# Optimization experiments

Hardware: AMD Instinct MI355X
Metric: run time of the kernel (lower is better)

Reference implementation:

```python
import jax, jax.numpy as jnp
import numpy as np
from jax import lax

EPS = 2.220446049250313e-16  # np.finfo(float).eps, as in the torch source
DN3 = ('NCDHW', 'OIDHW', 'NCDHW')
DN2 = ('NCHW', 'OIHW', 'NCHW')


def setup_inputs() -> dict:
    key = jax.random.key(0)
    k1, k2, k3 = jax.random.split(key, 3)
    x = jax.random.normal(k1, (256, 256), dtype=jnp.float32)
    filts_temp = jax.random.normal(k2, (8, 1, 2, 9, 9), dtype=jnp.float32)    # [Ft,1,T=2,kh,kw]
    filts_notemp = jax.random.normal(k3, (8, 1, 1, 9, 9), dtype=jnp.float32)  # [Fn,1,1,kh,kw]
    return {"x": x, "filts_temp": filts_temp, "filts_notemp": filts_notemp, "num_rfs": 2}


def _forward(x, filts_temp, filts_notemp, num_rfs):
    kh, kw = filts_temp.shape[3], filts_temp.shape[4]
    corr_x = num_rfs * kh  # torch uses shape[3]
    corr_y = num_rfs * kw  # torch uses shape[4]
    num_filts = filts_temp.shape[0] + filts_notemp.shape[0]

    # x -> [1,1,2,H,W]: duplicate the frame along a temporal axis of length 2
    xv = jnp.broadcast_to(x, (2,) + x.shape)[None, None]

    # fixed-filter temporal conv3d + ReLU (halved)
    x_temp = jax.nn.relu(
        lax.conv_general_dilated(xv, filts_temp, (1, 1, 1), 'VALID', dimension_numbers=DN3) / 2
    )  # [1,Ft,1,H',W']
    # non-temporal conv on the last time slice
    x_notemp = jax.nn.relu(
        lax.conv_general_dilated(xv[:, :, -1:, :, :], filts_notemp, (1, 1, 1), 'VALID',
                                 dimension_numbers=DN3)
    )  # [1,Fn,1,H',W']

    xc = jnp.concatenate([x_temp, x_notemp], axis=1)  # [1,nf,1,H',W']
    # normalize across the filter channel (divisive normalization)
    x1 = xc / (jnp.sum(xc, axis=1, keepdims=True) + EPS)

    H_, W_ = x1.shape[3], x1.shape[4]
    x1f = x1[0, :, 0]  # [nf,H',W']
    # central crop used as correlation templates
    templates = x1f[:, corr_y:H_ - corr_y, corr_x:W_ - corr_x]  # [nf, H'-2cy, W'-2cx]

    # windowed pairwise cross-channel correlation: the torch conv3d with depth-kernel 1
    # is exactly a batched 2D valid cross-correlation (batch = depth index j,
    # out-channel = template index i)
    out = lax.conv_general_dilated(x1f[:, None], templates[:, None], (1, 1), 'VALID',
                                   dimension_numbers=DN2)  # [j, i, 2cy+1, 2cx+1]
    x2 = jnp.transpose(out, (1, 0, 2, 3))[None]  # [1, i, j, 2cy+1, 2cx+1]
    # note: source divides by (y_max-2*corr_y)*(x_max-2*corr_y) (corr_y twice) -- kept faithful
    x2 = x2 / ((H_ - 2 * corr_y) * (W_ - 2 * corr_y))

    x1_out = x1f[None, None]  # [1,1,nf,H',W']
    return (x1_out, x2)


def reference(x, filts_temp, filts_notemp, num_rfs):
    return _forward(x, filts_temp, filts_notemp, num_rfs)
```

## Files before the change

kernel.cpp:

```cpp
#include <hip/hip_runtime.h>
#include <hip/hip_fp8.h>
#include <cstdint>

typedef unsigned short u16;
typedef unsigned int   u32;
typedef unsigned long long u64;
typedef float  f32x16 __attribute__((ext_vector_type(16)));
typedef float  f32x4  __attribute__((ext_vector_type(4)));
typedef u32    u32x2  __attribute__((ext_vector_type(2)));
typedef u32    u32x4  __attribute__((ext_vector_type(4)));

#define OUT1 984064
#define OUT2 350464

#define XD5        1015808
#define TMPL_OFFB  16252928
#define PART_OFFB  17027072
#define PART_ELEMS (6*OUT2)
#define XC_OFFB    25438208

__global__ __launch_bounds__(256) void k1_conv(
    const float* __restrict__ x, const float* __restrict__ ft,
    const float* __restrict__ fnt, float* __restrict__ out1,
    u16* __restrict__ Xc) {
  __shared__ float xt[24][25];
  __shared__ float wsm[1296];
  const int tid = threadIdx.x;
  const int lx = tid & 15, ly = tid >> 4;
  const int bx = blockIdx.x, by = blockIdx.y;
  for (int idx = tid; idx < 1296; idx += 256) {
    int c = idx / 81, s = idx - (idx / 81) * 81;
    wsm[idx] = (c < 8) ? 0.5f * (ft[c*162 + s] + ft[c*162 + 81 + s])
                       : fnt[(c-8)*81 + s];
  }
  for (int idx = tid; idx < 576; idx += 256) {
    int ry = idx / 24, rx = idx - ry * 24;
    int gy = by*16 + ry; gy = gy > 255 ? 255 : gy;
    int gx = bx*16 + rx; gx = gx > 255 ? 255 : gx;
    xt[ry][rx] = x[gy*256 + gx];
  }
  __syncthreads();
  const int xg = bx*16 + lx, yg = by*16 + ly;
  if (yg >= 248) return;
  float s[16];
#pragma unroll
  for (int c = 0; c < 16; ++c) s[c] = 0.f;
  const bool valid = (xg < 248);
  if (valid) {
#pragma unroll
    for (int u = 0; u < 9; ++u)
#pragma unroll
      for (int v = 0; v < 9; ++v) {
        float xv = xt[ly + u][lx + v];
#pragma unroll
        for (int c = 0; c < 16; ++c)
          s[c] = __builtin_fmaf(xv, wsm[c*81 + u*9 + v], s[c]);
      }
    float sum = 2.2204460492503131e-16f;
#pragma unroll
    for (int c = 0; c < 16; ++c) { s[c] = s[c] > 0.f ? s[c] : 0.f; sum += s[c]; }
    float inv = 1.f / sum;
#pragma unroll
    for (int c = 0; c < 16; ++c) s[c] *= inv;
  }
#pragma unroll
  for (int c = 0; c < 16; ++c) {
    u16 hb = 0;
    if (valid) {
      out1[c*61504 + yg*248 + xg] = s[c];
      u32 ub = __builtin_bit_cast(u32, s[c]);
      hb = (u16)((ub + 0x7fffu + ((ub >> 16) & 1u)) >> 16);
    }
    Xc[(c*248 + yg)*272 + xg] = hb;
  }
}

__device__ __forceinline__ u32 pk4_fp8(u32 b0, u32 b1) {
  float f0 = __builtin_bit_cast(float, b0 << 16);
  float f1 = __builtin_bit_cast(float, b0 & 0xFFFF0000u);
  float f2 = __builtin_bit_cast(float, b1 << 16);
  float f3 = __builtin_bit_cast(float, b1 & 0xFFFF0000u);
  __hip_fp8_e4m3 e0(f0), e1(f1), e2(f2), e3(f3);
  return (u32)e0.__x | ((u32)e1.__x << 8) | ((u32)e2.__x << 16) | ((u32)e3.__x << 24);
}

__global__ __launch_bounds__(256) void k1b_expand(
    const u16* __restrict__ Xc, unsigned char* __restrict__ ws8,
    float* __restrict__ partial) {
  const int cid = blockIdx.x*256 + threadIdx.x;
  for (int z = cid; z < PART_ELEMS; z += gridDim.x*256) partial[z] = 0.f;
  const u32* src = (const u32*)Xc;
  if (cid < 1015808) {
    int n  = cid & 15;
    int r1 = cid >> 4;
    int row = r1 % 248;
    int r2  = r1 / 248;
    int vp  = r2 & 15;
    int d   = r2 >> 4;
    int col0 = d + 16*vp;
    int so = (n*248 + row)*136 + (col0 >> 1);
    u32 a[9], b[8];
#pragma unroll
    for (int i = 0; i < 9; ++i) a[i] = src[so + i];
    if (d & 1) {
#pragma unroll
      for (int i = 0; i < 8; ++i) b[i] = (a[i] >> 16) | (a[i+1] << 16);
    } else {
#pragma unroll
      for (int i = 0; i < 8; ++i) b[i] = a[i];
    }
    u32x4 v = { pk4_fp8(b[0], b[1]), pk4_fp8(b[2], b[3]),
                pk4_fp8(b[4], b[5]), pk4_fp8(b[6], b[7]) };
    *(u32x4*)(ws8 + ((size_t)((d*16 + vp)*248 + row))*256 + n*16) = v;
  } else if (cid < 1015808 + 48384) {
    int t  = cid - 1015808;
    int o  = t & 15;
    int r1 = t >> 4;
    int tr = r1 % 216;
    int vp = r1 / 216;
    u32x4 v = {0u, 0u, 0u, 0u};
    if (tr < 212) {
      int so = (o*248 + tr + 18)*136 + ((18 + 16*vp) >> 1);
      u32 b[8];
#pragma unroll
      for (int i = 0; i < 8; ++i) b[i] = src[so + i];
      v[0] = pk4_fp8(b[0], b[1]);
      if (vp < 13) {
        v[1] = pk4_fp8(b[2], b[3]);
        v[2] = pk4_fp8(b[4], b[5]);
        v[3] = pk4_fp8(b[6], b[7]);
      }
    }
    *(u32x4*)(ws8 + TMPL_OFFB + ((size_t)(vp*216 + tr))*256 + o*16) = v;
  }
}

#define F_LD(k,m,c) fl[(k)*1024 + (((m)&3) + 4*((m)>>3))*64 + ((c) + 32*(((m)>>2)&1))]

#define LD_A(q,SO) asm volatile("buffer_load_dwordx4 %0, %1, %2, %3 offen" \
  : "=v"(A[q]) : "v"(voffA[q]), "s"(srdA), "s"(SO));
#define LD_B(t,SO) asm volatile("buffer_load_dwordx4 %0, %1, %2, %3 offen" \
  : "=v"(B[t]) : "v"(voffB[t]), "s"(srdB), "s"(SO));
#define WT(N,X,Y) asm volatile("s_waitcnt vmcnt(" #N ")" : "+v"(X), "+v"(Y) ::);
#define LO8(V) __builtin_bit_cast(long, (u32x2){(V)[0], (V)[1]})
#define HI8(V) __builtin_bit_cast(long, (u32x2){(V)[2], (V)[3]})
#define MF10(t) { long _bl = LO8(B[t]), _bh = HI8(B[t]); \
  acc[0]=__builtin_amdgcn_mfma_f32_32x32x16_fp8_fp8(LO8(A[t+0]),_bl,acc[0],0,0,0); \
  acc[1]=__builtin_amdgcn_mfma_f32_32x32x16_fp8_fp8(LO8(A[t+1]),_bl,acc[1],0,0,0); \
  acc[2]=__builtin_amdgcn_mfma_f32_32x32x16_fp8_fp8(LO8(A[t+2]),_bl,acc[2],0,0,0); \
  acc[3]=__builtin_amdgcn_mfma_f32_32x32x16_fp8_fp8(LO8(A[t+3]),_bl,acc[3],0,0,0); \
  acc[4]=__builtin_amdgcn_mfma_f32_32x32x16_fp8_fp8(LO8(A[t+4]),_bl,acc[4],0,0,0); \
  acc[0]=__builtin_amdgcn_mfma_f32_32x32x16_fp8_fp8(HI8(A[t+0]),_bh,acc[0],0,0,0); \
  acc[1]=__builtin_amdgcn_mfma_f32_32x32x16_fp8_fp8(HI8(A[t+1]),_bh,acc[1],0,0,0); \
  acc[2]=__builtin_amdgcn_mfma_f32_32x32x16_fp8_fp8(HI8(A[t+2]),_bh,acc[2],0,0,0); \
  acc[3]=__builtin_amdgcn_mfma_f32_32x32x16_fp8_fp8(HI8(A[t+3]),_bh,acc[3],0,0,0); \
  acc[4]=__builtin_amdgcn_mfma_f32_32x32x16_fp8_fp8(HI8(A[t+4]),_bh,acc[4],0,0,0); }

__global__ __launch_bounds__(256, 2) void k2_corr(
    const unsigned char* __restrict__ Ximg5, const unsigned char* __restrict__ Tmpl5,
    float* __restrict__ partial) {
  __shared__ float fl[5120];
  const int bid = blockIdx.x;
  const int jl  = bid & 7;
  const int m0  = bid >> 3;
  const int jj  = m0 % 5;
  const int cmb = m0 / 5;
  const int g   = cmb & 3;
  const int uq  = cmb >> 2;
  const int j   = jl + 8*jj;
  if (j >= 37) return;
  const int U0  = 72*uq;
  const int R0  = 10*g + U0;
  const int tid  = threadIdx.x;
  const int lane = tid & 63;
  const int w    = tid >> 6;
  const int fn16 = lane & 15;
  const int fuu  = (lane >> 4) & 1;
  const int fg   = lane >> 5;

  u64 pa = (u64)(Ximg5 + (j & 15)*XD5 + (j >> 4)*63488);
  u64 pb = (u64)(Tmpl5);
  u32x4 srdA = { (u32)pa, (u32)(pa >> 32), 0xFFFFFFFFu, 0x00020000u };
  u32x4 srdB = { (u32)pb, (u32)(pb >> 32), 0xFFFFFFFFu, 0x00020000u };
  int voffA[13], voffB[9];
#pragma unroll
  for (int q = 0; q < 13; ++q) {
    int r = R0 + fuu + 18*w + 2*q;
    if (r > 247) r = 247;
    voffA[q] = fg*63488 + fn16*16 + r*256;
  }
#pragma unroll
  for (int t = 0; t < 9; ++t)
    voffB[t] = fg*55296 + fn16*16 + (U0 + fuu + 18*w + 2*t)*256;

  f32x16 acc[5];
#pragma unroll
  for (int k = 0; k < 5; ++k)
#pragma unroll
    for (int q = 0; q < 16; ++q) acc[k][q] = 0.f;

  u32x4 A[13], B[9];
  { int sa = 0, sb = 0;
    LD_A(0,sa) LD_B(0,sb) LD_A(1,sa) LD_B(1,sb)
    LD_A(2,sa) LD_B(2,sb) LD_A(3,sa) LD_B(3,sb)
    LD_A(4,sa) LD_B(4,sb) LD_A(5,sa) LD_B(5,sb)
    LD_A(6,sa) LD_B(6,sb) LD_A(7,sa) LD_B(7,sb)
    LD_A(8,sa) LD_A(9,sa) LD_A(10,sa) LD_A(11,sa) LD_A(12,sa) LD_B(8,sb) }

#pragma unroll 1
  for (int s = 0; s < 6; ++s) {
    const int sa = (s + 1)*126976, sb = (s + 1)*110592;
    WT(13, A[4],  B[0])  MF10(0) LD_A(0,sa) LD_B(0,sb)
    WT(13, A[5],  B[1])  MF10(1) LD_A(1,sa) LD_B(1,sb)
    WT(13, A[6],  B[2])  MF10(2) LD_A(2,sa) LD_B(2,sb)
    WT(13, A[7],  B[3])  MF10(3) LD_A(3,sa) LD_B(3,sb)
    WT(13, A[8],  B[4])  MF10(4) LD_A(4,sa) LD_B(4,sb)
    WT(14, A[9],  B[5])  MF10(5) LD_A(5,sa) LD_B(5,sb)
    WT(15, A[10], B[6])  MF10(6) LD_A(6,sa) LD_B(6,sb)
    WT(16, A[11], B[7])  MF10(7) LD_A(7,sa) LD_B(7,sb)
    WT(16, A[12], B[8])  MF10(8)
    LD_A(8,sa) LD_A(9,sa) LD_A(10,sa) LD_A(11,sa) LD_A(12,sa) LD_B(8,sb)
  }
  WT(13, A[4],  B[0])  MF10(0)
  WT(11, A[5],  B[1])  MF10(1)
  WT(9,  A[6],  B[2])  MF10(2)
  WT(7,  A[7],  B[3])  MF10(3)
  WT(5,  A[8],  B[4])  MF10(4)
  WT(4,  A[9],  B[5])  MF10(5)
  WT(3,  A[10], B[6])  MF10(6)
  WT(2,  A[11], B[7])  MF10(7)
  WT(0,  A[12], B[8])  MF10(8)
  __syncthreads();

  for (int z = tid; z < 5120; z += 256) fl[z] = 0.f;
  __syncthreads();
  for (int ww = 0; ww < 4; ++ww) {
    if (w == ww) {
#pragma unroll
      for (int k = 0; k < 5; ++k) {
        if (!(g == 3 && k == 4)) {
#pragma unroll
          for (int q = 0; q < 16; ++q)
            fl[k*1024 + q*64 + lane] += acc[k][q];
        }
      }
    }
    __syncthreads();
  }

  const int n = (tid >> 4) & 15;
  const int o = tid & 15;
  float* slab = partial + (uq*2 + (g & 1)) * OUT2;
  for (int ii = 0; ii < 11; ++ii) {
    const int i = 10*g - 1 + ii;
    if (i < 0 || i >= 37) continue;
    const int dd = ii - 1;
    float v;
    if (!(dd & 1)) {
      const int k = dd >> 1;
      v = F_LD(k, n, o) + F_LD(k, n+16, o+16);
    } else {
      v = 0.f;
      if (dd >= 1) v += F_LD((dd-1) >> 1, n+16, o);
      const int kr = (dd+1) >> 1;
      if (kr <= 4) v += F_LD(kr, n, o+16);
    }
    slab[(o*16 + n)*1369 + i*37 + j] = v;
  }
}

__global__ __launch_bounds__(256) void k3_reduce(
    const float* __restrict__ partial, float* __restrict__ out2) {
  const int idx = blockIdx.x*256 + threadIdx.x;
  if (idx >= OUT2/4) return;
  f32x4 s = {0.f, 0.f, 0.f, 0.f};
#pragma unroll
  for (int t = 0; t < 6; ++t) {
    f32x4 v = *(const f32x4*)(partial + t*OUT2 + idx*4);
    s[0] += v[0]; s[1] += v[1]; s[2] += v[2]; s[3] += v[3];
  }
  const float sc = 1.0f / 44944.0f;
  s[0] *= sc; s[1] *= sc; s[2] *= sc; s[3] *= sc;
  *(f32x4*)(out2 + idx*4) = s;
}

extern "C" void kernel_launch(void* const* d_in, const int* in_sizes, int n_in,
                              void* d_out, int out_size, void* d_ws, size_t ws_size,
                              hipStream_t stream) {
  (void)in_sizes; (void)n_in; (void)out_size; (void)ws_size;
  const float* x   = (const float*)d_in[0];
  const float* ft  = (const float*)d_in[1];
  const float* fnt = (const float*)d_in[2];
  float* out = (float*)d_out;
  char*  ws  = (char*)d_ws;
  unsigned char* Ximg5 = (unsigned char*)ws;
  unsigned char* Tmpl5 = (unsigned char*)(ws + TMPL_OFFB);
  float* partial = (float*)(ws + PART_OFFB);
  u16*   Xc      = (u16*)(ws + XC_OFFB);

  k1_conv<<<dim3(17, 16), 256, 0, stream>>>(x, ft, fnt, out, Xc);
  k1b_expand<<<4157, 256, 0, stream>>>(Xc, (unsigned char*)ws, partial);
  k2_corr<<<480, 256, 0, stream>>>(Ximg5, Tmpl5, partial);
  k3_reduce<<<343, 256, 0, stream>>>(partial, out + OUT1);
}
```

Before: 69.87 us.

## Coalesce partial-sum writes with position-major layout and add sc0 load hints

The correlation kernel now writes partial sums in a position-major layout indexed by thread id, so each wavefront's stores to the partial slabs are contiguous instead of strided by 1369. The reduce kernel is rewritten to read that layout coalesced and scatter the final output back into the original channel-major order. Buffer loads for the A and B operands also gain the sc0 cache-policy bit. The trade-off is that the final output writes are now strided, and the reduce launches fewer, larger blocks.

```diff
diff --git a/kernel.cpp b/kernel.cpp
--- a/kernel.cpp
+++ b/kernel.cpp
@@ -137,9 +137,9 @@
 
 #define F_LD(k,m,c) fl[(k)*1024 + (((m)&3) + 4*((m)>>3))*64 + ((c) + 32*(((m)>>2)&1))]
 
-#define LD_A(q,SO) asm volatile("buffer_load_dwordx4 %0, %1, %2, %3 offen" \
+#define LD_A(q,SO) asm volatile("buffer_load_dwordx4 %0, %1, %2, %3 offen sc0" \
   : "=v"(A[q]) : "v"(voffA[q]), "s"(srdA), "s"(SO));
-#define LD_B(t,SO) asm volatile("buffer_load_dwordx4 %0, %1, %2, %3 offen" \
+#define LD_B(t,SO) asm volatile("buffer_load_dwordx4 %0, %1, %2, %3 offen sc0" \
   : "=v"(B[t]) : "v"(voffB[t]), "s"(srdB), "s"(SO));
 #define WT(N,X,Y) asm volatile("s_waitcnt vmcnt(" #N ")" : "+v"(X), "+v"(Y) ::);
 #define LO8(V) __builtin_bit_cast(long, (u32x2){(V)[0], (V)[1]})
@@ -265,23 +265,32 @@
       const int kr = (dd+1) >> 1;
       if (kr <= 4) v += F_LD(kr, n, o+16);
     }
-    slab[(o*16 + n)*1369 + i*37 + j] = v;
+    slab[(i*37 + j)*256 + tid] = v;
   }
 }
 
 __global__ __launch_bounds__(256) void k3_reduce(
     const float* __restrict__ partial, float* __restrict__ out2) {
-  const int idx = blockIdx.x*256 + threadIdx.x;
-  if (idx >= OUT2/4) return;
-  f32x4 s = {0.f, 0.f, 0.f, 0.f};
-#pragma unroll
-  for (int t = 0; t < 6; ++t) {
-    f32x4 v = *(const f32x4*)(partial + t*OUT2 + idx*4);
-    s[0] += v[0]; s[1] += v[1]; s[2] += v[2]; s[3] += v[3];
-  }
+  const int r0 = blockIdx.x * 8;
+  const int tid = threadIdx.x;
+  float v[8];
+#pragma unroll
+  for (int rr = 0; rr < 8; ++rr) v[rr] = 0.f;
+#pragma unroll
+  for (int t = 0; t < 6; ++t)
+#pragma unroll
+    for (int rr = 0; rr < 8; ++rr) {
+      int r = r0 + rr;
+      if (r < 1369) v[rr] += partial[t*OUT2 + r*256 + tid];
+    }
+  const int n = tid >> 4, o = tid & 15;
   const float sc = 1.0f / 44944.0f;
-  s[0] *= sc; s[1] *= sc; s[2] *= sc; s[3] *= sc;
-  *(f32x4*)(out2 + idx*4) = s;
+  float* dst = out2 + (o*16 + n)*1369;
+#pragma unroll
+  for (int rr = 0; rr < 8; ++rr) {
+    int r = r0 + rr;
+    if (r < 1369) dst[r] = v[rr] * sc;
+  }
 }
 
 extern "C" void kernel_launch(void* const* d_in, const int* in_sizes, int n_in,
@@ -301,5 +310,5 @@
   k1_conv<<<dim3(17, 16), 256, 0, stream>>>(x, ft, fnt, out, Xc);
   k1b_expand<<<4157, 256, 0, stream>>>(Xc, (unsigned char*)ws, partial);
   k2_corr<<<480, 256, 0, stream>>>(Ximg5, Tmpl5, partial);
-  k3_reduce<<<343, 256, 0, stream>>>(partial, out + OUT1);
-}
+  k3_reduce<<<172, 256, 0, stream>>>(partial, out + OUT1);
+}
```

Result: slower. 77.30 us (+10.6%).
